# Kernel optimization log

Hardware: AMD Instinct MI355X
Metric: run time of the kernel (lower is better)

## Reference

```python
import jax, jax.numpy as jnp
import numpy as np

B, N, M, K, D = 8, 100000, 2048, 32, 128
EPS = 1e-5


def setup_inputs() -> dict:
    key = jax.random.key(0)
    ks = jax.random.split(key, 10)
    return dict(
        point_feat=jax.random.normal(ks[0], (B, N, D), jnp.float32),
        point_xyz=jax.random.normal(ks[1], (B, N, 3), jnp.float32),
        supernode_xyz=jax.random.normal(ks[2], (B, M, 3), jnp.float32),
        neighbor_idx=jax.random.randint(ks[3], (B, M, K), 0, N),
        neighbor_mask=jax.random.randint(ks[4], (B, M, K), 0, 2).astype(bool),
        supernode_init_feat=jax.random.normal(ks[5], (B, M, D), jnp.float32),
        task_emb=jax.random.normal(ks[6], (B, D), jnp.float32),
        W1=jax.random.normal(ks[7], (D + 4, D), jnp.float32) * 0.05,
        b1=jnp.zeros((D,), jnp.float32),
        W2=jax.random.normal(ks[8], (D, D), jnp.float32) * 0.05,
        b2=jnp.zeros((D,), jnp.float32),
        Wf=jax.random.normal(ks[9], (D, 2 * D), jnp.float32) * 0.02,  # FiLM head (identity-ish init)
        bf=jnp.zeros((2 * D,), jnp.float32),
        ln_g=jnp.ones((D,), jnp.float32),
        ln_b=jnp.zeros((D,), jnp.float32),
    )


def reference(point_feat, point_xyz, supernode_xyz, neighbor_idx, neighbor_mask,
              supernode_init_feat, task_emb, W1, b1, W2, b2, Wf, bf, ln_g, ln_b):
    # batched neighbor gather: [B,M,K] indices into [B,N,*]
    gather = jax.vmap(lambda feats, idx: feats[idx])
    neigh_feat = gather(point_feat, neighbor_idx)            # [B,M,K,D]
    neigh_xyz = gather(point_xyz, neighbor_idx)              # [B,M,K,3]
    rel = neigh_xyz - supernode_xyz[:, :, None, :]           # [B,M,K,3]
    dist = jnp.linalg.norm(rel, axis=-1, keepdims=True)      # [B,M,K,1]
    x = jnp.concatenate([neigh_feat, rel, dist], axis=-1)    # [B,M,K,D+4]
    msg = jax.nn.silu(x @ W1 + b1) @ W2 + b2                 # [B,M,K,D]
    # masked mean over neighbors, denom clamped to >= 1
    mask_f = neighbor_mask.astype(msg.dtype)[..., None]      # [B,M,K,1]
    agg = (msg * mask_f).sum(axis=2) / jnp.maximum(mask_f.sum(axis=2), 1.0)  # [B,M,D]
    # task FiLM: x * (1 + gamma) + beta
    gamma, beta = jnp.split(task_emb @ Wf + bf, 2, axis=-1)  # each [B,D]
    agg = agg * (1.0 + gamma[:, None, :]) + beta[:, None, :]
    # residual + LayerNorm
    h = supernode_init_feat + agg
    mu = h.mean(axis=-1, keepdims=True)
    var = ((h - mu) ** 2).mean(axis=-1, keepdims=True)
    return (h - mu) * jax.lax.rsqrt(var + EPS) * ln_g + ln_b
```

## Files before the change

kernel.cpp:

```cpp
#include <hip/hip_runtime.h>
#include <hip/hip_bf16.h>

#define B_ 8
#define N_ 100000
#define M_ 2048
#define K_ 32
#define D_ 128
#define KP 160
#define EPS_ 1e-5f

typedef __attribute__((ext_vector_type(8))) short bf16x8;
typedef __attribute__((ext_vector_type(4))) float f32x4;

__device__ __forceinline__ short f2bf(float f) {
    unsigned int u = __builtin_bit_cast(unsigned int, f);
    u += 0x7fffu + ((u >> 16) & 1u);
    return (short)(u >> 16);
}
__device__ __forceinline__ float bf2f(short s) {
    unsigned int u = ((unsigned int)(unsigned short)s) << 16;
    return __builtin_bit_cast(float, u);
}

__global__ __launch_bounds__(256) void prep_kernel(
    const float* __restrict__ W1, const float* __restrict__ b1,
    const float* __restrict__ task_emb, const float* __restrict__ Wf,
    const float* __restrict__ bfv,
    short* __restrict__ w1t, float* __restrict__ gb)
{
    if (blockIdx.x == 0) {
        for (int e = threadIdx.x; e < 128 * KP; e += 256) {
            const int n = e / KP;
            const int k = e - n * KP;
            float v = 0.f;
            if (k < 132) v = W1[k * 128 + n];
            else if (k == 132) v = b1[n];
            w1t[e] = f2bf(v);
        }
    } else {
        const int b = blockIdx.x - 1;
        const int col = threadIdx.x;
        float acc = bfv[col];
        for (int i = 0; i < 128; ++i) acc += task_emb[b * 128 + i] * Wf[i * 256 + col];
        gb[b * 256 + col] = acc;
    }
}

__global__ __launch_bounds__(256) void msg_kernel(
    const float* __restrict__ point_feat,
    const float* __restrict__ point_xyz,
    const float* __restrict__ supernode_xyz,
    const int*   __restrict__ nidx,
    const int*   __restrict__ nmask,
    const short* __restrict__ w1t,
    float* __restrict__ agg_out,
    float* __restrict__ cflag)
{
    const int lane = threadIdx.x & 63;
    const int wave = threadIdx.x >> 6;
    const int sm = blockIdx.x * 4 + wave;
    const int b  = sm >> 11;
    const int c  = lane & 15;
    const int q  = lane >> 4;
    const long base_bm = (long)sm * K_;

    const int idx0 = nidx[base_bm + c];
    const int idx1 = nidx[base_bm + 16 + c];

    const bool mv = (lane < K_) && (nmask[base_bm + lane] != 0);
    const unsigned long long bal = __ballot(mv);
    const int cnt = __popcll(bal);
    const float inv_d = 1.0f / (float)(cnt > 0 ? cnt : 1);

    const float* sxp = supernode_xyz + (long)sm * 3;
    const float sx = sxp[0], sy = sxp[1], sz = sxp[2];

    union U { bf16x8 v; short s[8]; };

    U a4[2];
    {
        const int idxs[2] = { idx0, idx1 };
        #pragma unroll
        for (int tt = 0; tt < 2; ++tt) {
            U u;
            #pragma unroll
            for (int jj = 0; jj < 8; ++jj) u.s[jj] = 0;
            if (q == 0) {
                const float* p = point_xyz + ((long)b * N_ + idxs[tt]) * 3;
                const float rx = p[0] - sx, ry = p[1] - sy, rz = p[2] - sz;
                const float dd = sqrtf(rx * rx + ry * ry + rz * rz);
                u.s[0] = f2bf(rx); u.s[1] = f2bf(ry); u.s[2] = f2bf(rz);
                u.s[3] = f2bf(dd); u.s[4] = f2bf(1.0f);
            }
            a4[tt] = u;
        }
    }

    const f32x4 zero = { 0.f, 0.f, 0.f, 0.f };
    f32x4 acc[2][8];
    #pragma unroll
    for (int mt = 0; mt < 2; ++mt)
        #pragma unroll
        for (int nt = 0; nt < 8; ++nt) acc[mt][nt] = zero;

    const float* featb = point_feat + (long)b * N_ * D_;
    const float* prow0 = featb + (long)idx0 * D_ + q * 8;
    const float* prow1 = featb + (long)idx1 * D_ + q * 8;
    const short* wbase = w1t + c * KP + q * 8;

    #pragma unroll
    for (int ks = 0; ks < 4; ++ks) {
        bf16x8 bfr[8];
        #pragma unroll
        for (int nt = 0; nt < 8; ++nt)
            bfr[nt] = *reinterpret_cast<const bf16x8*>(wbase + nt * 16 * KP + ks * 32);
        U ua0, ua1;
        {
            const f32x4 x0 = *reinterpret_cast<const f32x4*>(prow0 + ks * 32);
            const f32x4 x1 = *reinterpret_cast<const f32x4*>(prow0 + ks * 32 + 4);
            const f32x4 y0 = *reinterpret_cast<const f32x4*>(prow1 + ks * 32);
            const f32x4 y1 = *reinterpret_cast<const f32x4*>(prow1 + ks * 32 + 4);
            #pragma unroll
            for (int jj = 0; jj < 4; ++jj) {
                ua0.s[jj] = f2bf(x0[jj]); ua0.s[4 + jj] = f2bf(x1[jj]);
                ua1.s[jj] = f2bf(y0[jj]); ua1.s[4 + jj] = f2bf(y1[jj]);
            }
        }
        #pragma unroll
        for (int nt = 0; nt < 8; ++nt) {
            acc[0][nt] = __builtin_amdgcn_mfma_f32_16x16x32_bf16(ua0.v, bfr[nt], acc[0][nt], 0, 0, 0);
            acc[1][nt] = __builtin_amdgcn_mfma_f32_16x16x32_bf16(ua1.v, bfr[nt], acc[1][nt], 0, 0, 0);
        }
    }
    #pragma unroll
    for (int nt = 0; nt < 8; ++nt) {
        const bf16x8 bfr = *reinterpret_cast<const bf16x8*>(wbase + nt * 16 * KP + 4 * 32);
        acc[0][nt] = __builtin_amdgcn_mfma_f32_16x16x32_bf16(a4[0].v, bfr, acc[0][nt], 0, 0, 0);
        acc[1][nt] = __builtin_amdgcn_mfma_f32_16x16x32_bf16(a4[1].v, bfr, acc[1][nt], 0, 0, 0);
    }

    #pragma unroll
    for (int nt = 0; nt < 8; ++nt) {
        float part = 0.f;
        #pragma unroll
        for (int mt = 0; mt < 2; ++mt) {
            #pragma unroll
            for (int r = 0; r < 4; ++r) {
                const int row = mt * 16 + q * 4 + r;
                const float v = acc[mt][nt][r];
                const float s = v / (1.0f + __expf(-v));
                part += ((bal >> row) & 1ULL) ? s : 0.0f;
            }
        }
        part += __shfl_xor(part, 16);
        part += __shfl_xor(part, 32);
        if (q == 0) agg_out[(long)sm * D_ + nt * 16 + c] = part * inv_d;
    }
    if (lane == 0) cflag[sm] = (cnt > 0) ? 1.0f : 0.0f;
}

__global__ __launch_bounds__(256) void out_kernel(
    float* __restrict__ inout,
    const float* __restrict__ W2,
    const float* __restrict__ b2,
    const float* __restrict__ cflag,
    const float* __restrict__ gb,
    const float* __restrict__ init_feat,
    const float* __restrict__ ln_g,
    const float* __restrict__ ln_b)
{
    __shared__ short sW2[128 * 128];
    __shared__ float sA[128];
    __shared__ float sPart[256];
    __shared__ float sRed[8];

    const int t = threadIdx.x;
    for (int i = t; i < 128 * 128; i += 256) sW2[i] = f2bf(W2[i]);

    const int j = t & 127;
    const int p = t >> 7;
    const int s0 = blockIdx.x * 16;
    __syncthreads();

    for (int si = 0; si < 16; ++si) {
        const int s = s0 + si;
        if (t < 128) sA[t] = inout[(long)s * D_ + t];
        __syncthreads();
        float partial = 0.f;
        #pragma unroll 8
        for (int i = p * 64; i < p * 64 + 64; ++i)
            partial += sA[i] * bf2f(sW2[i * 128 + j]);
        sPart[t] = partial;
        __syncthreads();
        const int b = s >> 11;
        float h = 0.f;
        if (t < 128) {
            const float msg = sPart[j] + sPart[128 + j] + cflag[s] * b2[j];
            const float g  = gb[b * 256 + j];
            const float be = gb[b * 256 + 128 + j];
            const float v = msg * (1.f + g) + be;
            h = init_feat[(long)s * D_ + j] + v;
        }
        float a1 = h, a2 = h * h;
        #pragma unroll
        for (int off = 32; off > 0; off >>= 1) {
            a1 += __shfl_xor(a1, off);
            a2 += __shfl_xor(a2, off);
        }
        if ((t & 63) == 0) { sRed[t >> 6] = a1; sRed[4 + (t >> 6)] = a2; }
        __syncthreads();
        const float mu  = (sRed[0] + sRed[1]) * (1.f / 128.f);
        const float var = (sRed[4] + sRed[5]) * (1.f / 128.f) - mu * mu;
        if (t < 128) {
            const float o = (h - mu) * rsqrtf(var + EPS_) * ln_g[j] + ln_b[j];
            inout[(long)s * D_ + j] = o;
        }
        __syncthreads();
    }
}

extern "C" void kernel_launch(void* const* d_in, const int* in_sizes, int n_in,
                              void* d_out, int out_size, void* d_ws, size_t ws_size,
                              hipStream_t stream) {
    const float* point_feat     = (const float*)d_in[0];
    const float* point_xyz      = (const float*)d_in[1];
    const float* supernode_xyz  = (const float*)d_in[2];
    const int*   neighbor_idx   = (const int*)d_in[3];
    const int*   neighbor_mask  = (const int*)d_in[4];
    const float* supernode_init = (const float*)d_in[5];
    const float* task_emb       = (const float*)d_in[6];
    const float* W1             = (const float*)d_in[7];
    const float* b1             = (const float*)d_in[8];
    const float* W2             = (const float*)d_in[9];
    const float* b2             = (const float*)d_in[10];
    const float* Wf             = (const float*)d_in[11];
    const float* bfv            = (const float*)d_in[12];
    const float* ln_g           = (const float*)d_in[13];
    const float* ln_b           = (const float*)d_in[14];

    char* ws = (char*)d_ws;
    short* w1t  = (short*)ws;
    float* gb   = (float*)(ws + 40960);
    float* cfl  = (float*)(ws + 49152);
    float* out  = (float*)d_out;

    prep_kernel<<<9, 256, 0, stream>>>(W1, b1, task_emb, Wf, bfv, w1t, gb);
    msg_kernel<<<(B_ * M_) / 4, 256, 0, stream>>>(point_feat, point_xyz, supernode_xyz,
                                                  neighbor_idx, neighbor_mask, w1t, out, cfl);
    out_kernel<<<(B_ * M_) / 16, 256, 0, stream>>>(out, W2, b2, cfl, gb,
                                                   supernode_init, ln_g, ln_b);
}
```

Before: 668.1 us.

## Skip masked neighbor gathers, stage W1 in LDS, MFMA second projection

The message kernel now stages the padded bf16 W1 into shared memory once per block and skips the point-feature and xyz gathers for masked-out neighbors, which cuts random global traffic roughly in half for this mask. The output kernel replaces the scalar per-supernode W2 matvec loop, which used many block barriers, with a bf16 MFMA tile of 16 supernodes per wave. The pre-transposed W2 comes from the prep kernel, and LayerNorm uses wave shuffles. In exchange the message kernel uses about 43KB of LDS per block, which may limit occupancy.

```diff
diff --git a/kernel.cpp b/kernel.cpp
--- a/kernel.cpp
+++ b/kernel.cpp
@@ -6,7 +6,8 @@
 #define M_ 2048
 #define K_ 32
 #define D_ 128
-#define KP 160
+#define KPL 168
+#define KL2 136
 #define EPS_ 1e-5f
 
 typedef __attribute__((ext_vector_type(8))) short bf16x8;
@@ -17,28 +18,31 @@
     u += 0x7fffu + ((u >> 16) & 1u);
     return (short)(u >> 16);
 }
-__device__ __forceinline__ float bf2f(short s) {
-    unsigned int u = ((unsigned int)(unsigned short)s) << 16;
-    return __builtin_bit_cast(float, u);
-}
 
 __global__ __launch_bounds__(256) void prep_kernel(
     const float* __restrict__ W1, const float* __restrict__ b1,
+    const float* __restrict__ W2,
     const float* __restrict__ task_emb, const float* __restrict__ Wf,
     const float* __restrict__ bfv,
-    short* __restrict__ w1t, float* __restrict__ gb)
+    short* __restrict__ w1t, short* __restrict__ w2t, float* __restrict__ gb)
 {
     if (blockIdx.x == 0) {
-        for (int e = threadIdx.x; e < 128 * KP; e += 256) {
-            const int n = e / KP;
-            const int k = e - n * KP;
+        for (int e = threadIdx.x; e < 128 * KPL; e += 256) {
+            const int n = e / KPL;
+            const int k = e - n * KPL;
             float v = 0.f;
             if (k < 132) v = W1[k * 128 + n];
             else if (k == 132) v = b1[n];
             w1t[e] = f2bf(v);
         }
+    } else if (blockIdx.x == 1) {
+        for (int e = threadIdx.x; e < 128 * KL2; e += 256) {
+            const int n = e / KL2;
+            const int k = e - n * KL2;
+            w2t[e] = f2bf(k < 128 ? W2[k * 128 + n] : 0.f);
+        }
     } else {
-        const int b = blockIdx.x - 1;
+        const int b = blockIdx.x - 2;
         const int col = threadIdx.x;
         float acc = bfv[col];
         for (int i = 0; i < 128; ++i) acc += task_emb[b * 128 + i] * Wf[i * 256 + col];
@@ -56,6 +60,15 @@
     float* __restrict__ agg_out,
     float* __restrict__ cflag)
 {
+    __shared__ short sw[128 * KPL];
+    {
+        const uint2* src = (const uint2*)w1t;
+        uint2* dst = (uint2*)sw;
+        #pragma unroll
+        for (int i = 0; i < 21; ++i) dst[threadIdx.x + i * 256] = src[threadIdx.x + i * 256];
+    }
+    __syncthreads();
+
     const int lane = threadIdx.x & 63;
     const int wave = threadIdx.x >> 6;
     const int sm = blockIdx.x * 4 + wave;
@@ -71,6 +84,8 @@
     const unsigned long long bal = __ballot(mv);
     const int cnt = __popcll(bal);
     const float inv_d = 1.0f / (float)(cnt > 0 ? cnt : 1);
+    const bool v0 = (bal >> c) & 1ULL;
+    const bool v1 = (bal >> (16 + c)) & 1ULL;
 
     const float* sxp = supernode_xyz + (long)sm * 3;
     const float sx = sxp[0], sy = sxp[1], sz = sxp[2];
@@ -80,12 +95,13 @@
     U a4[2];
     {
         const int idxs[2] = { idx0, idx1 };
+        const bool vs[2] = { v0, v1 };
         #pragma unroll
         for (int tt = 0; tt < 2; ++tt) {
             U u;
             #pragma unroll
             for (int jj = 0; jj < 8; ++jj) u.s[jj] = 0;
-            if (q == 0) {
+            if (q == 0 && vs[tt]) {
                 const float* p = point_xyz + ((long)b * N_ + idxs[tt]) * 3;
                 const float rx = p[0] - sx, ry = p[1] - sy, rz = p[2] - sz;
                 const float dd = sqrtf(rx * rx + ry * ry + rz * rz);
@@ -106,25 +122,26 @@
     const float* featb = point_feat + (long)b * N_ * D_;
     const float* prow0 = featb + (long)idx0 * D_ + q * 8;
     const float* prow1 = featb + (long)idx1 * D_ + q * 8;
-    const short* wbase = w1t + c * KP + q * 8;
+    const short* wb = sw + c * KPL + q * 8;
 
     #pragma unroll
     for (int ks = 0; ks < 4; ++ks) {
         bf16x8 bfr[8];
         #pragma unroll
         for (int nt = 0; nt < 8; ++nt)
-            bfr[nt] = *reinterpret_cast<const bf16x8*>(wbase + nt * 16 * KP + ks * 32);
-        U ua0, ua1;
-        {
+            bfr[nt] = *reinterpret_cast<const bf16x8*>(wb + nt * 16 * KPL + ks * 32);
+        U ua0 = {}, ua1 = {};
+        if (v0) {
             const f32x4 x0 = *reinterpret_cast<const f32x4*>(prow0 + ks * 32);
             const f32x4 x1 = *reinterpret_cast<const f32x4*>(prow0 + ks * 32 + 4);
+            #pragma unroll
+            for (int jj = 0; jj < 4; ++jj) { ua0.s[jj] = f2bf(x0[jj]); ua0.s[4 + jj] = f2bf(x1[jj]); }
+        }
+        if (v1) {
             const f32x4 y0 = *reinterpret_cast<const f32x4*>(prow1 + ks * 32);
             const f32x4 y1 = *reinterpret_cast<const f32x4*>(prow1 + ks * 32 + 4);
             #pragma unroll
-            for (int jj = 0; jj < 4; ++jj) {
-                ua0.s[jj] = f2bf(x0[jj]); ua0.s[4 + jj] = f2bf(x1[jj]);
-                ua1.s[jj] = f2bf(y0[jj]); ua1.s[4 + jj] = f2bf(y1[jj]);
-            }
+            for (int jj = 0; jj < 4; ++jj) { ua1.s[jj] = f2bf(y0[jj]); ua1.s[4 + jj] = f2bf(y1[jj]); }
         }
         #pragma unroll
         for (int nt = 0; nt < 8; ++nt) {
@@ -134,7 +151,7 @@
     }
     #pragma unroll
     for (int nt = 0; nt < 8; ++nt) {
-        const bf16x8 bfr = *reinterpret_cast<const bf16x8*>(wbase + nt * 16 * KP + 4 * 32);
+        const bf16x8 bfr = *reinterpret_cast<const bf16x8*>(wb + nt * 16 * KPL + 4 * 32);
         acc[0][nt] = __builtin_amdgcn_mfma_f32_16x16x32_bf16(a4[0].v, bfr, acc[0][nt], 0, 0, 0);
         acc[1][nt] = __builtin_amdgcn_mfma_f32_16x16x32_bf16(a4[1].v, bfr, acc[1][nt], 0, 0, 0);
     }
@@ -161,7 +178,7 @@
 
 __global__ __launch_bounds__(256) void out_kernel(
     float* __restrict__ inout,
-    const float* __restrict__ W2,
+    const short* __restrict__ w2t,
     const float* __restrict__ b2,
     const float* __restrict__ cflag,
     const float* __restrict__ gb,
@@ -169,53 +186,82 @@
     const float* __restrict__ ln_g,
     const float* __restrict__ ln_b)
 {
-    __shared__ short sW2[128 * 128];
-    __shared__ float sA[128];
-    __shared__ float sPart[256];
-    __shared__ float sRed[8];
-
-    const int t = threadIdx.x;
-    for (int i = t; i < 128 * 128; i += 256) sW2[i] = f2bf(W2[i]);
-
-    const int j = t & 127;
-    const int p = t >> 7;
-    const int s0 = blockIdx.x * 16;
+    __shared__ short sw[128 * KL2];
+    {
+        const uint2* src = (const uint2*)w2t;
+        uint2* dst = (uint2*)sw;
+        #pragma unroll
+        for (int i = 0; i < 17; ++i) dst[threadIdx.x + i * 256] = src[threadIdx.x + i * 256];
+    }
     __syncthreads();
 
-    for (int si = 0; si < 16; ++si) {
-        const int s = s0 + si;
-        if (t < 128) sA[t] = inout[(long)s * D_ + t];
-        __syncthreads();
-        float partial = 0.f;
-        #pragma unroll 8
-        for (int i = p * 64; i < p * 64 + 64; ++i)
-            partial += sA[i] * bf2f(sW2[i * 128 + j]);
-        sPart[t] = partial;
-        __syncthreads();
-        const int b = s >> 11;
-        float h = 0.f;
-        if (t < 128) {
-            const float msg = sPart[j] + sPart[128 + j] + cflag[s] * b2[j];
-            const float g  = gb[b * 256 + j];
-            const float be = gb[b * 256 + 128 + j];
-            const float v = msg * (1.f + g) + be;
-            h = init_feat[(long)s * D_ + j] + v;
-        }
-        float a1 = h, a2 = h * h;
-        #pragma unroll
-        for (int off = 32; off > 0; off >>= 1) {
-            a1 += __shfl_xor(a1, off);
-            a2 += __shfl_xor(a2, off);
-        }
-        if ((t & 63) == 0) { sRed[t >> 6] = a1; sRed[4 + (t >> 6)] = a2; }
-        __syncthreads();
-        const float mu  = (sRed[0] + sRed[1]) * (1.f / 128.f);
-        const float var = (sRed[4] + sRed[5]) * (1.f / 128.f) - mu * mu;
-        if (t < 128) {
-            const float o = (h - mu) * rsqrtf(var + EPS_) * ln_g[j] + ln_b[j];
-            inout[(long)s * D_ + j] = o;
-        }
-        __syncthreads();
+    const int lane = threadIdx.x & 63;
+    const int wave = threadIdx.x >> 6;
+    const int s0 = blockIdx.x * 64 + wave * 16;
+    const int b  = s0 >> 11;
+    const int c  = lane & 15;
+    const int q  = lane >> 4;
+
+    union U { bf16x8 v; short s[8]; };
+    const f32x4 zero = { 0.f, 0.f, 0.f, 0.f };
+    f32x4 acc[8];
+    #pragma unroll
+    for (int nt = 0; nt < 8; ++nt) acc[nt] = zero;
+
+    const float* arow = inout + (long)(s0 + c) * D_ + q * 8;
+    const short* wb = sw + c * KL2 + q * 8;
+
+    #pragma unroll
+    for (int ks = 0; ks < 4; ++ks) {
+        U ua;
+        {
+            const f32x4 x0 = *reinterpret_cast<const f32x4*>(arow + ks * 32);
+            const f32x4 x1 = *reinterpret_cast<const f32x4*>(arow + ks * 32 + 4);
+            #pragma unroll
+            for (int jj = 0; jj < 4; ++jj) { ua.s[jj] = f2bf(x0[jj]); ua.s[4 + jj] = f2bf(x1[jj]); }
+        }
+        #pragma unroll
+        for (int nt = 0; nt < 8; ++nt) {
+            const bf16x8 bfr = *reinterpret_cast<const bf16x8*>(wb + nt * 16 * KL2 + ks * 32);
+            acc[nt] = __builtin_amdgcn_mfma_f32_16x16x32_bf16(ua.v, bfr, acc[nt], 0, 0, 0);
+        }
+    }
+
+    float gv[8], bev[8], b2v[8], lgv[8], lbv[8];
+    #pragma unroll
+    for (int nt = 0; nt < 8; ++nt) {
+        const int col = nt * 16 + c;
+        gv[nt]  = gb[b * 256 + col];
+        bev[nt] = gb[b * 256 + 128 + col];
+        b2v[nt] = b2[col];
+        lgv[nt] = ln_g[col];
+        lbv[nt] = ln_b[col];
+    }
+
+    #pragma unroll
+    for (int r = 0; r < 4; ++r) {
+        const int row = s0 + q * 4 + r;
+        const float cf = cflag[row];
+        float h[8];
+        float s1 = 0.f, s2 = 0.f;
+        #pragma unroll
+        for (int nt = 0; nt < 8; ++nt) {
+            const float msgv = acc[nt][r] + cf * b2v[nt];
+            const float v = msgv * (1.f + gv[nt]) + bev[nt];
+            const float hh = init_feat[(long)row * D_ + nt * 16 + c] + v;
+            h[nt] = hh; s1 += hh; s2 += hh * hh;
+        }
+        #pragma unroll
+        for (int off = 1; off < 16; off <<= 1) {
+            s1 += __shfl_xor(s1, off);
+            s2 += __shfl_xor(s2, off);
+        }
+        const float mu = s1 * (1.f / 128.f);
+        const float var = s2 * (1.f / 128.f) - mu * mu;
+        const float rs = rsqrtf(var + EPS_);
+        #pragma unroll
+        for (int nt = 0; nt < 8; ++nt)
+            inout[(long)row * D_ + nt * 16 + c] = (h[nt] - mu) * rs * lgv[nt] + lbv[nt];
     }
 }
 
@@ -240,13 +286,14 @@
 
     char* ws = (char*)d_ws;
     short* w1t  = (short*)ws;
-    float* gb   = (float*)(ws + 40960);
-    float* cfl  = (float*)(ws + 49152);
+    short* w2t  = (short*)(ws + 44032);
+    float* gb   = (float*)(ws + 78848);
+    float* cfl  = (float*)(ws + 87040);
     float* out  = (float*)d_out;
 
-    prep_kernel<<<9, 256, 0, stream>>>(W1, b1, task_emb, Wf, bfv, w1t, gb);
+    prep_kernel<<<10, 256, 0, stream>>>(W1, b1, W2, task_emb, Wf, bfv, w1t, w2t, gb);
     msg_kernel<<<(B_ * M_) / 4, 256, 0, stream>>>(point_feat, point_xyz, supernode_xyz,
                                                   neighbor_idx, neighbor_mask, w1t, out, cfl);
-    out_kernel<<<(B_ * M_) / 16, 256, 0, stream>>>(out, W2, b2, cfl, gb,
+    out_kernel<<<(B_ * M_) / 64, 256, 0, stream>>>(out, w2t, b2, cfl, gb,
                                                    supernode_init, ln_g, ln_b);
 }
```

After: 590.7 us. 11.6% less time.
